# Kernel tuning notes

Measured on AMD Instinct MI355X. Metric: run time of the kernel, lower is better.

## Reference

```python
import jax, jax.numpy as jnp
import numpy as np

H, C = 4, 128            # GATConv heads, per-head out channels
MAX_NODES, NF = 50, 64   # generator graph size, node feature dim
N_NODES, N_EDGES, N_GRAPHS, LAT, HID = 10000, 160000, 64, 64, 128


def _p(key, i, shape):
    return jax.random.normal(jax.random.fold_in(key, i), shape, jnp.float32) * 0.05


def setup_inputs() -> dict:
    key = jax.random.key(0)
    inp = {}
    inp['x'] = jax.random.normal(jax.random.fold_in(key, 0), (N_NODES, NF), jnp.float32)
    inp['edge_index'] = jax.random.randint(jax.random.fold_in(key, 1), (2, N_EDGES), 0, N_NODES)
    inp['batch'] = jnp.sort(jax.random.randint(jax.random.fold_in(key, 2), (N_NODES,), 0, N_GRAPHS))
    inp['eps'] = jax.random.normal(jax.random.fold_in(key, 3), (N_GRAPHS, LAT), jnp.float32)
    # encoder params
    inp['We'] = _p(key, 10, (NF, HID)); inp['be'] = _p(key, 11, (HID,))
    inp['Wg'] = _p(key, 12, (3, HID, H * C))
    inp['ag_src'] = _p(key, 13, (3, H, C)); inp['ag_dst'] = _p(key, 14, (3, H, C))
    inp['bg'] = _p(key, 15, (3, C))
    inp['Wa1'] = _p(key, 16, (HID, 2 * HID)); inp['ba1'] = _p(key, 17, (2 * HID,))
    inp['Wa2'] = _p(key, 18, (2 * HID, HID)); inp['ba2'] = _p(key, 19, (HID,))
    inp['Wmu'] = _p(key, 20, (HID, LAT)); inp['bmu'] = _p(key, 21, (LAT,))
    inp['Wlv'] = _p(key, 22, (HID, LAT)); inp['blv'] = _p(key, 23, (LAT,))
    # generator params
    inp['Wn1'] = _p(key, 30, (LAT, 256)); inp['bn1'] = _p(key, 31, (256,))
    inp['Wn2'] = _p(key, 32, (256, 512)); inp['bn2'] = _p(key, 33, (512,))
    inp['Wn3'] = _p(key, 34, (512, MAX_NODES * NF)); inp['bn3'] = _p(key, 35, (MAX_NODES * NF,))
    inp['We1'] = _p(key, 36, (LAT + 2 * NF, 128)); inp['be1'] = _p(key, 37, (128,))
    inp['We2'] = _p(key, 38, (128, 64)); inp['be2'] = _p(key, 39, (64,))
    inp['We3'] = _p(key, 40, (64, 1)); inp['be3'] = _p(key, 41, (1,))
    inp['Wr1'] = _p(key, 42, (2 * NF, 64)); inp['br1'] = _p(key, 43, (64,))
    inp['Wr2'] = _p(key, 44, (64, 6)); inp['br2'] = _p(key, 45, (6,))
    return inp


def _gat(h, W, a_s, a_d, b, src, dst, N):
    # PyG GATConv: heads=4, concat=False (mean over heads), neg_slope=0.2, self-loops pre-added
    xh = (h @ W).reshape(N, H, C)                      # [N,H,C]
    es = (xh * a_s[None]).sum(-1)                      # [N,H] alpha_src component
    ed = (xh * a_d[None]).sum(-1)                      # [N,H] alpha_dst component
    e = jax.nn.leaky_relu(es[src] + ed[dst], 0.2)      # [E,H]
    m = jax.ops.segment_max(e, dst, num_segments=N)
    ex = jnp.exp(e - m[dst])
    den = jax.ops.segment_sum(ex, dst, num_segments=N)
    alpha = ex / den[dst]                              # softmax over incoming edges
    out = jax.ops.segment_sum(xh[src] * alpha[:, :, None], dst, num_segments=N)
    return out.mean(axis=1) + b                        # mean over heads + bias


def reference(x, eps, We, be, Wg, ag_src, ag_dst, bg, Wa1, ba1, Wa2, ba2,
              Wmu, bmu, Wlv, blv, Wn1, bn1, Wn2, bn2, Wn3, bn3,
              We1, be1, We2, be2, We3, be3, Wr1, br1, Wr2, br2,
              edge_index, batch):
    N = x.shape[0]
    B = eps.shape[0]
    loops = jnp.arange(N)
    src = jnp.concatenate([edge_index[0], loops])
    dst = jnp.concatenate([edge_index[1], loops])
    # PathwayEncoder
    h = jax.nn.relu(x @ We + be)
    for l in range(3):
        h = h + jax.nn.relu(_gat(h, Wg[l], ag_src[l], ag_dst[l], bg[l], src, dst, N))
    counts = jax.ops.segment_sum(jnp.ones((N,), h.dtype), batch, num_segments=B)
    sums = jax.ops.segment_sum(h, batch, num_segments=B)
    pr = sums / jnp.maximum(counts, 1.0)[:, None]      # global_mean_pool
    pr = jax.nn.relu(pr @ Wa1 + ba1) @ Wa2 + ba2       # pathway_aggregator
    # VAE head
    mu = pr @ Wmu + bmu
    logvar = pr @ Wlv + blv
    z = mu + eps * jnp.exp(0.5 * logvar)
    # PathwayGenerator (pairwise loop fully batched)
    g = jax.nn.relu(z @ Wn1 + bn1)
    g = jax.nn.relu(g @ Wn2 + bn2)
    nodes = (g @ Wn3 + bn3).reshape(B, MAX_NODES, NF)  # node_features (pre-sigmoid)
    node_probs = jax.nn.sigmoid(nodes)
    iu, ju = np.triu_indices(MAX_NODES, k=1)           # 1225 static pairs (i<j)
    ni = nodes[:, iu]                                  # [B,P,NF]
    nj = nodes[:, ju]
    P = iu.shape[0]
    zb = jnp.broadcast_to(z[:, None, :], (B, P, z.shape[-1]))
    eh = jax.nn.relu(jnp.concatenate([zb, ni, nj], -1) @ We1 + be1)
    eh = jax.nn.relu(eh @ We2 + be2)
    edge_probs = jax.nn.sigmoid(eh @ We3 + be3)[..., 0]            # [B,P]
    rh = jax.nn.relu(jnp.concatenate([ni, nj], -1) @ Wr1 + br1)
    reaction_types = jax.nn.softmax(rh @ Wr2 + br2, axis=-1)       # [B,P,6]
    return (mu, logvar, z, pr, node_probs, edge_probs, reaction_types)
```

## Files before the change

### kernel.cpp

```cpp
#include <hip/hip_runtime.h>
#include <cstddef>

#define N_NODES 10000
#define N_EDGES 160000
#define E_TOT   170000
#define N_GRAPHS 64
#define NF 64
#define HID 128
#define HC 512
#define LAT 64
#define MAXN 50
#define NPAIR 1225
#define NODESF 3200
#define DEG_CAP 64

typedef __attribute__((ext_vector_type(8))) short bf16x8;
typedef __attribute__((ext_vector_type(8))) unsigned short u16x8;
typedef __attribute__((ext_vector_type(4))) float f32x4;
typedef unsigned short u16;
typedef unsigned int u32;

__device__ __forceinline__ u16 f2b(float f) {
    u32 u = __float_as_uint(f);
    u32 r = (u + 0x7fffu + ((u >> 16) & 1u)) >> 16;
    return (u16)r;
}
__device__ __forceinline__ float b2f(u16 v) {
    return __uint_as_float(((u32)v) << 16);
}

struct PackArgs {
    const float* src[15];
    u16* dst[15];
};
#define PACK_TOTAL 344192
#define PACK_GRID_TOTAL (PACK_TOTAL + NPAIR + E_TOT)
__global__ void pack_all_kernel(PackArgs pa, int* __restrict__ pi, int* __restrict__ pj,
                                const int* __restrict__ ei, int* __restrict__ cursor,
                                int* __restrict__ csr_src) {
    int idx = blockIdx.x * 256 + threadIdx.x;
    if (idx >= PACK_GRID_TOTAL) return;
    if (idx >= PACK_TOTAL) {
        int r = idx - PACK_TOTAL;
        if (r < NPAIR) {
            int i = 0, off = 0;
            while (off + (MAXN - 1 - i) <= r) { off += MAXN - 1 - i; ++i; }
            pi[r] = i;
            pj[r] = i + 1 + (r - off);
        } else {
            int e = r - NPAIR;
            int s, d;
            if (e < N_EDGES) { s = ei[e]; d = ei[N_EDGES + e]; }
            else { s = e - N_EDGES; d = s; }
            int pos = atomicAdd(&cursor[d], 1);
            csr_src[(d << 6) + pos] = s;
        }
        return;
    }
    const int base[16] = {0, 8192, 16384, 24576, 27648, 28672, 29696, 33792, 37888,
                          38912, 39936, 41984, 58368, 263168, 264192, 344192};
    const int Ns[15]   = {512, 512, 512, 128, 64, 64, 256, 128, 64, 64, 256, 512, 3200, 128, 0};
    const int dNs[15]  = {512, 512, 512, 128, 64, 64, 256, 128, 128, 128, 256, 512, 3200, 128, 0};
    const int coff[15] = {0, 0, 0, 0, 0, 0, 0, 0, 0, 64, 0, 0, 0, 0, 0};
    int s = 0;
    while (idx >= base[s + 1]) ++s;
    int i = idx - base[s];
    const float* sp = pa.src[s];
    u16* dp = pa.dst[s];
    if (s == 14) {
        u16x8 o;
#pragma unroll
        for (int j = 0; j < 8; ++j) o[j] = f2b(sp[(size_t)i * 8 + j]);
        *(u16x8*)&dp[(size_t)i * 8] = o;
        return;
    }
    int N = Ns[s];
    int g = i / N, n = i - g * N;
    u16x8 o;
#pragma unroll
    for (int j = 0; j < 8; ++j) o[j] = f2b(sp[(size_t)(g * 8 + j) * N + n]);
    *(u16x8*)&dp[((size_t)g * dNs[s] + n + coff[s]) * 8] = o;
}

template<int K, int NT, int CB, bool BIAS, bool RELU, bool F32OUT>
__global__ __launch_bounds__(256) void gemm_mh_kernel(const u16* __restrict__ A,
                                                      const u16* __restrict__ Wp,
                                                      const float* __restrict__ bias,
                                                      u16* __restrict__ bo,
                                                      float* __restrict__ fo) {
    constexpr int CT = CB / 64;
    __shared__ u16 AL[64 * (K + 8)];
    int t = threadIdx.x, w = t >> 6, l = t & 63, lr = l & 15, lg = l >> 4;
    int rb = blockIdx.x * 64, j0 = blockIdx.y * CB;
    for (int u = t; u < 64 * (K / 8); u += 256) {
        int r = u / (K / 8), c8 = (u % (K / 8)) * 8;
        int row = min(rb + r, N_NODES - 1);
        *(u16x8*)&AL[r * (K + 8) + c8] = *(const u16x8*)&A[(size_t)row * K + c8];
    }
    __syncthreads();
    f32x4 acc[4][CT];
#pragma unroll
    for (int rt = 0; rt < 4; ++rt)
#pragma unroll
        for (int ct = 0; ct < CT; ++ct) acc[rt][ct] = (f32x4){0.f, 0.f, 0.f, 0.f};
#pragma unroll
    for (int ks = 0; ks < K / 32; ++ks) {
        bf16x8 a[4], b[CT];
#pragma unroll
        for (int rt = 0; rt < 4; ++rt)
            a[rt] = *(const bf16x8*)&AL[(rt * 16 + lr) * (K + 8) + ks * 32 + lg * 8];
#pragma unroll
        for (int ct = 0; ct < CT; ++ct) {
            int col = j0 + w * (CB / 4) + ct * 16 + lr;
            b[ct] = *(const bf16x8*)&Wp[(size_t)((ks * 4 + lg) * NT + col) * 8];
        }
#pragma unroll
        for (int rt = 0; rt < 4; ++rt)
#pragma unroll
            for (int ct = 0; ct < CT; ++ct)
                acc[rt][ct] = __builtin_amdgcn_mfma_f32_16x16x32_bf16(a[rt], b[ct], acc[rt][ct], 0, 0, 0);
    }
#pragma unroll
    for (int rt = 0; rt < 4; ++rt)
#pragma unroll
        for (int ct = 0; ct < CT; ++ct) {
            int col = j0 + w * (CB / 4) + ct * 16 + lr;
            float bj = BIAS ? bias[col] : 0.f;
#pragma unroll
            for (int i = 0; i < 4; ++i) {
                int row = rb + rt * 16 + lg * 4 + i;
                if (row < N_NODES) {
                    float v = acc[rt][ct][i] + bj;
                    if (RELU) v = fmaxf(v, 0.f);
                    bo[(size_t)row * NT + col] = f2b(v);
                    if (F32OUT) fo[(size_t)row * NT + col] = v;
                }
            }
        }
}

template<int K, int G, int ACT, bool SPLIT>
__global__ __launch_bounds__(256) void gemm64_kernel(const u16* __restrict__ A,
                                                     const u16* __restrict__ Wp,
                                                     const float* __restrict__ bias,
                                                     const float* __restrict__ bias2,
                                                     float* __restrict__ fo,
                                                     float* __restrict__ fo2,
                                                     u16* __restrict__ bo, int N) {
    constexpr int CG = 4 / G, NB = CG * 16, Kc = K / G, KS = Kc / 32;
    constexpr int ABYTES = 64 * (K + 8) * 2;
    constexpr int LDSB = (ABYTES > 16384) ? ABYTES : 16384;
    __shared__ float LDSf[LDSB / 4];
    u16* AL = (u16*)LDSf;
    float* RB = LDSf;
    int t = threadIdx.x, w = t >> 6, l = t & 63, lr = l & 15, lg = l >> 4;
    for (int u = t; u < 64 * (K / 8); u += 256) {
        int r = u / (K / 8), c8 = (u % (K / 8)) * 8;
        *(u16x8*)&AL[r * (K + 8) + c8] = *(const u16x8*)&A[(size_t)r * K + c8];
    }
    __syncthreads();
    int kg = w % G, cg = w / G;
    int col = blockIdx.x * NB + cg * 16 + lr;
    f32x4 acc[4];
#pragma unroll
    for (int rt = 0; rt < 4; ++rt) acc[rt] = (f32x4){0.f, 0.f, 0.f, 0.f};
#pragma unroll
    for (int ks = 0; ks < KS; ++ks) {
        int k0 = kg * Kc + ks * 32;
        bf16x8 b = *(const bf16x8*)&Wp[(size_t)(((k0 >> 3) + lg) * N + col) * 8];
#pragma unroll
        for (int rt = 0; rt < 4; ++rt) {
            bf16x8 a = *(const bf16x8*)&AL[(rt * 16 + lr) * (K + 8) + k0 + lg * 8];
            acc[rt] = __builtin_amdgcn_mfma_f32_16x16x32_bf16(a, b, acc[rt], 0, 0, 0);
        }
    }
    __syncthreads();
#pragma unroll
    for (int rt = 0; rt < 4; ++rt)
#pragma unroll
        for (int i = 0; i < 4; ++i)
            RB[w * 1024 + (rt * 16 + lg * 4 + i) * 16 + lr] = acc[rt][i];
    __syncthreads();
    for (int e = t; e < 64 * NB; e += 256) {
        int row = e / NB, cb = e - row * NB;
        int cg2 = cb >> 4, cl = cb & 15;
        float s = 0.f;
#pragma unroll
        for (int kg2 = 0; kg2 < G; ++kg2)
            s += RB[(cg2 * G + kg2) * 1024 + row * 16 + cl];
        int c = blockIdx.x * NB + cb;
        float bj;
        if (SPLIT) bj = (c < 64) ? bias[c] : bias2[c - 64];
        else bj = bias[c];
        float v = s + bj;
        if (ACT == 1) v = fmaxf(v, 0.f);
        if (bo) bo[(size_t)row * N + c] = f2b(v);
        if (SPLIT) {
            if (c < 64) fo[row * 64 + c] = v;
            else fo2[row * 64 + (c - 64)] = v;
        } else if (fo) {
            float ov = (ACT == 2) ? 1.f / (1.f + __expf(-v)) : v;
            fo[(size_t)row * N + c] = ov;
        }
    }
}

template<int K, int N, typename EP>
__device__ __forceinline__ void mm64(const u16* __restrict__ AL, int lda,
                                     const u16* __restrict__ Wp, EP ep) {
    int t = threadIdx.x, w = t >> 6, l = t & 63, lr = l & 15, lg = l >> 4;
#pragma unroll
    for (int p = 0; p < N / 64; ++p) {
        int col = p * 64 + w * 16 + lr;
        f32x4 acc[4];
#pragma unroll
        for (int rt = 0; rt < 4; ++rt) acc[rt] = (f32x4){0.f, 0.f, 0.f, 0.f};
#pragma unroll
        for (int ks = 0; ks < K / 32; ++ks) {
            bf16x8 b = *(const bf16x8*)&Wp[(size_t)((ks * 4 + lg) * N + col) * 8];
#pragma unroll
            for (int rt = 0; rt < 4; ++rt) {
                bf16x8 a = *(const bf16x8*)&AL[(rt * 16 + lr) * lda + ks * 32 + lg * 8];
                acc[rt] = __builtin_amdgcn_mfma_f32_16x16x32_bf16(a, b, acc[rt], 0, 0, 0);
            }
        }
#pragma unroll
        for (int rt = 0; rt < 4; ++rt)
#pragma unroll
            for (int i = 0; i < 4; ++i)
                ep(rt * 16 + lg * 4 + i, col, acc[rt][i]);
    }
}

__global__ __launch_bounds__(256) void fused_vae_kernel(
    const u16* __restrict__ pr0b, const float* __restrict__ eps,
    const u16* __restrict__ Wa1p, const float* __restrict__ ba1,
    const u16* __restrict__ Wa2p, const float* __restrict__ ba2,
    const u16* __restrict__ Wmulvp, const float* __restrict__ bmu, const float* __restrict__ blv,
    const u16* __restrict__ Wn1p, const float* __restrict__ bn1,
    const u16* __restrict__ Wn2p, const float* __restrict__ bn2,
    float* __restrict__ pr_o, float* __restrict__ mu_o, float* __restrict__ lv_o,
    float* __restrict__ z_o, u16* __restrict__ zbf, u16* __restrict__ g2bb) {
    __shared__ u16 P[64 * 136];
    __shared__ u16 T[64 * 272];
    __shared__ u16 Z[64 * 72];
    float* MVf = (float*)T;
    int t = threadIdx.x;
    for (int idx = t; idx < 8192; idx += 256) {
        int g = idx >> 7, c = idx & 127;
        P[g * 136 + c] = pr0b[idx];
    }
    __syncthreads();
    mm64<128, 256>(P, 136, Wa1p, [&](int row, int col, float v) {
        T[row * 272 + col] = f2b(fmaxf(v + ba1[col], 0.f));
    });
    __syncthreads();
    mm64<256, 128>(T, 272, Wa2p, [&](int row, int col, float v) {
        v += ba2[col];
        pr_o[row * 128 + col] = v;
        P[row * 136 + col] = f2b(v);
    });
    __syncthreads();
    mm64<128, 128>(P, 136, Wmulvp, [&](int row, int col, float v) {
        v += (col < 64) ? bmu[col] : blv[col - 64];
        MVf[row * 136 + col] = v;
        if (col < 64) mu_o[row * 64 + col] = v;
        else lv_o[row * 64 + (col - 64)] = v;
    });
    __syncthreads();
    for (int idx = t; idx < 4096; idx += 256) {
        int g = idx >> 6, c = idx & 63;
        float m = MVf[g * 136 + c], lvv = MVf[g * 136 + 64 + c];
        float zv = fmaf(eps[idx], __expf(0.5f * lvv), m);
        z_o[idx] = zv;
        u16 zb16 = f2b(zv);
        zbf[idx] = zb16;
        Z[g * 72 + c] = zb16;
    }
    __syncthreads();
    mm64<64, 256>(Z, 72, Wn1p, [&](int row, int col, float v) {
        T[row * 272 + col] = f2b(fmaxf(v + bn1[col], 0.f));
    });
    __syncthreads();
    mm64<256, 512>(T, 272, Wn2p, [&](int row, int col, float v) {
        g2bb[row * 512 + col] = f2b(fmaxf(v + bn2[col], 0.f));
    });
}

__global__ void esed_kernel(const u16* __restrict__ xhb, const float* __restrict__ ags,
                            const float* __restrict__ agd, float* __restrict__ es,
                            float* __restrict__ ed) {
    int wv = threadIdx.x >> 6, lane = threadIdx.x & 63;
    int n = blockIdx.x * 4 + wv;
    if (n >= N_NODES) return;
    u16x8 v = *(const u16x8*)&xhb[(size_t)n * 512 + lane * 8];
    float ps = 0.f, pd = 0.f;
#pragma unroll
    for (int j = 0; j < 8; ++j) {
        float f = b2f(v[j]);
        ps = fmaf(f, ags[lane * 8 + j], ps);
        pd = fmaf(f, agd[lane * 8 + j], pd);
    }
#pragma unroll
    for (int off = 1; off < 16; off <<= 1) {
        ps += __shfl_xor(ps, off);
        pd += __shfl_xor(pd, off);
    }
    if ((lane & 15) == 0) {
        es[n * 4 + (lane >> 4)] = ps;
        ed[n * 4 + (lane >> 4)] = pd;
    }
}

__global__ __launch_bounds__(256) void gat_agg_kernel(const u16* __restrict__ xhb,
                               const float* __restrict__ es, const float* __restrict__ ed,
                               const int* __restrict__ cursor, const int* __restrict__ csr_src,
                               const float* __restrict__ bg, float* __restrict__ h,
                               u16* __restrict__ hb) {
    __shared__ float aL[4][64][4];
    __shared__ int sL[4][64];
    int wv = threadIdx.x >> 6, lane = threadIdx.x & 63;
    int n = blockIdx.x * 4 + wv;
    int deg = cursor[n];
    const float4 ed4 = ((const float4*)ed)[n];
    const float edh[4] = {ed4.x, ed4.y, ed4.z, ed4.w};
    float ex0 = 0.f, ex1 = 0.f, ex2 = 0.f, ex3 = 0.f;
    if (lane < deg) {
        int sj = csr_src[(n << 6) + lane];
        sL[wv][lane] = sj;
        const float4 e4 = ((const float4*)es)[sj];
        const float ev[4] = {e4.x, e4.y, e4.z, e4.w};
        float exv[4];
#pragma unroll
        for (int hh = 0; hh < 4; ++hh) {
            float e = ev[hh] + edh[hh];
            e = e > 0.f ? e : 0.2f * e;
            e = fminf(e, 80.f);
            exv[hh] = __expf(e);
        }
        *(float4*)&aL[wv][lane][0] = make_float4(exv[0], exv[1], exv[2], exv[3]);
        ex0 = exv[0]; ex1 = exv[1]; ex2 = exv[2]; ex3 = exv[3];
    }
#pragma unroll
    for (int off = 32; off; off >>= 1) {
        ex0 += __shfl_xor(ex0, off);
        ex1 += __shfl_xor(ex1, off);
        ex2 += __shfl_xor(ex2, off);
        ex3 += __shfl_xor(ex3, off);
    }
    __syncthreads();
    int head = lane >> 4, c0 = (lane & 15) * 8;
    float den = (head == 0) ? ex0 : (head == 1) ? ex1 : (head == 2) ? ex2 : ex3;
    float acc[8] = {0.f, 0.f, 0.f, 0.f, 0.f, 0.f, 0.f, 0.f};
    const u16* xb_h = xhb + head * 128 + c0;
    int j2 = 0;
    for (; j2 + 2 <= deg; j2 += 2) {
        int s0 = sL[wv][j2], s1 = sL[wv][j2 + 1];
        float al0 = aL[wv][j2][head], al1 = aL[wv][j2 + 1][head];
        u16x8 v0 = *(const u16x8*)&xb_h[(size_t)s0 * 512];
        u16x8 v1 = *(const u16x8*)&xb_h[(size_t)s1 * 512];
#pragma unroll
        for (int m = 0; m < 8; ++m) acc[m] = fmaf(al0, b2f(v0[m]), acc[m]);
#pragma unroll
        for (int m = 0; m < 8; ++m) acc[m] = fmaf(al1, b2f(v1[m]), acc[m]);
    }
    if (j2 < deg) {
        int s0 = sL[wv][j2];
        float al0 = aL[wv][j2][head];
        u16x8 v0 = *(const u16x8*)&xb_h[(size_t)s0 * 512];
#pragma unroll
        for (int m = 0; m < 8; ++m) acc[m] = fmaf(al0, b2f(v0[m]), acc[m]);
    }
    float rden = 1.f / den;
#pragma unroll
    for (int m = 0; m < 8; ++m) {
        float v = acc[m] * rden;
        v += __shfl_xor(v, 16);
        v += __shfl_xor(v, 32);
        acc[m] = v;
    }
    if (lane < 16) {
        float o8[8];
        u16x8 b8;
#pragma unroll
        for (int m = 0; m < 8; ++m) {
            int c = lane * 8 + m;
            float o = acc[m] * 0.25f + bg[c];
            o = fmaxf(o, 0.f);
            float hn = h[(size_t)n * 128 + c] + o;
            o8[m] = hn;
            b8[m] = f2b(hn);
        }
        *(float4*)&h[(size_t)n * 128 + lane * 8] = make_float4(o8[0], o8[1], o8[2], o8[3]);
        *(float4*)&h[(size_t)n * 128 + lane * 8 + 4] = make_float4(o8[4], o8[5], o8[6], o8[7]);
        *(u16x8*)&hb[(size_t)n * 128 + lane * 8] = b8;
    }
}

__global__ __launch_bounds__(1024) void pool_kernel2(const float* __restrict__ h,
                                                     const int* __restrict__ batch,
                                                     u16* __restrict__ pr0b) {
    __shared__ float red[8][128];
    int g = blockIdx.x;
    int t = threadIdx.x;
    int c = t & 127, rg = t >> 7;
    int lo = 0, hi = N_NODES;
    while (lo < hi) { int m = (lo + hi) >> 1; if (batch[m] < g) lo = m + 1; else hi = m; }
    int s = lo;
    lo = 0; hi = N_NODES;
    while (lo < hi) { int m = (lo + hi) >> 1; if (batch[m] < g + 1) lo = m + 1; else hi = m; }
    int e = lo;
    float acc = 0.f;
    for (int n = s + rg; n < e; n += 8) acc += h[(size_t)n * HID + c];
    red[rg][c] = acc;
    __syncthreads();
    if (rg == 0) {
        float sum = ((red[0][c] + red[1][c]) + (red[2][c] + red[3][c])) +
                    ((red[4][c] + red[5][c]) + (red[6][c] + red[7][c]));
        float cn = fmaxf((float)(e - s), 1.f);
        pr0b[g * HID + c] = f2b(sum / cn);
    }
}

__global__ __launch_bounds__(256) void edge_react_mfma(
    const u16* __restrict__ zb, const u16* __restrict__ nb,
    const int* __restrict__ pi, const int* __restrict__ pj,
    const u16* __restrict__ We1p, const float* __restrict__ be1,
    const u16* __restrict__ We2p, const float* __restrict__ be2,
    const float* __restrict__ We3, const float* __restrict__ be3,
    const u16* __restrict__ Wr1p, const float* __restrict__ br1,
    const float* __restrict__ Wr2, const float* __restrict__ br2,
    float* __restrict__ edgep, float* __restrict__ react) {
    __shared__ u16 inA[64 * 200];
    __shared__ u16 h1A[64 * 136];
    __shared__ u16 rhA[64 * 68];
    int t = threadIdx.x, w = t >> 6, l = t & 63, lr = l & 15, lg = l >> 4;
    int b = blockIdx.y, p0 = blockIdx.x * 64;
    for (int u = t; u < 1536; u += 256) {
        int r = u / 24, c8 = (u % 24) * 8;
        int p = min(p0 + r, NPAIR - 1);
        const u16* src;
        if (c8 < 64) src = zb + b * 64 + c8;
        else if (c8 < 128) src = nb + b * NODESF + pi[p] * 64 + (c8 - 64);
        else src = nb + b * NODESF + pj[p] * 64 + (c8 - 128);
        *(u16x8*)&inA[r * 200 + c8] = *(const u16x8*)src;
    }
    __syncthreads();
    f32x4 a1[4][2];
#pragma unroll
    for (int rt = 0; rt < 4; ++rt)
#pragma unroll
        for (int ct = 0; ct < 2; ++ct) a1[rt][ct] = (f32x4){0.f, 0.f, 0.f, 0.f};
#pragma unroll
    for (int ks = 0; ks < 6; ++ks) {
        bf16x8 af[4], bf_[2];
#pragma unroll
        for (int rt = 0; rt < 4; ++rt)
            af[rt] = *(const bf16x8*)&inA[(rt * 16 + lr) * 200 + ks * 32 + lg * 8];
#pragma unroll
        for (int ct = 0; ct < 2; ++ct) {
            int col = w * 32 + ct * 16 + lr;
            bf_[ct] = *(const bf16x8*)&We1p[(size_t)((ks * 4 + lg) * 128 + col) * 8];
        }
#pragma unroll
        for (int rt = 0; rt < 4; ++rt)
#pragma unroll
            for (int ct = 0; ct < 2; ++ct)
                a1[rt][ct] = __builtin_amdgcn_mfma_f32_16x16x32_bf16(af[rt], bf_[ct], a1[rt][ct], 0, 0, 0);
    }
    f32x4 r1[4];
#pragma unroll
    for (int rt = 0; rt < 4; ++rt) r1[rt] = (f32x4){0.f, 0.f, 0.f, 0.f};
#pragma unroll
    for (int ks = 0; ks < 4; ++ks) {
        bf16x8 af[4];
#pragma unroll
        for (int rt = 0; rt < 4; ++rt)
            af[rt] = *(const bf16x8*)&inA[(rt * 16 + lr) * 200 + 64 + ks * 32 + lg * 8];
        int col = w * 16 + lr;
        bf16x8 bf_ = *(const bf16x8*)&Wr1p[(size_t)((ks * 4 + lg) * 64 + col) * 8];
#pragma unroll
        for (int rt = 0; rt < 4; ++rt)
            r1[rt] = __builtin_amdgcn_mfma_f32_16x16x32_bf16(af[rt], bf_, r1[rt], 0, 0, 0);
    }
#pragma unroll
    for (int rt = 0; rt < 4; ++rt)
#pragma unroll
        for (int ct = 0; ct < 2; ++ct) {
            int col = w * 32 + ct * 16 + lr;
            float bia = be1[col];
#pragma unroll
            for (int i = 0; i < 4; ++i) {
                int row = rt * 16 + lg * 4 + i;
                h1A[row * 136 + col] = f2b(fmaxf(a1[rt][ct][i] + bia, 0.f));
            }
        }
#pragma unroll
    for (int rt = 0; rt < 4; ++rt) {
        int col = w * 16 + lr;
        float bia = br1[col];
#pragma unroll
        for (int i = 0; i < 4; ++i) {
            int row = rt * 16 + lg * 4 + i;
            rhA[row * 68 + col] = f2b(fmaxf(r1[rt][i] + bia, 0.f));
        }
    }
    __syncthreads();
    f32x4 a2[4];
#pragma unroll
    for (int rt = 0; rt < 4; ++rt) a2[rt] = (f32x4){0.f, 0.f, 0.f, 0.f};
#pragma unroll
    for (int ks = 0; ks < 4; ++ks) {
        bf16x8 af[4];
#pragma unroll
        for (int rt = 0; rt < 4; ++rt)
            af[rt] = *(const bf16x8*)&h1A[(rt * 16 + lr) * 136 + ks * 32 + lg * 8];
        int col = w * 16 + lr;
        bf16x8 bf_ = *(const bf16x8*)&We2p[(size_t)((ks * 4 + lg) * 64 + col) * 8];
#pragma unroll
        for (int rt = 0; rt < 4; ++rt)
            a2[rt] = __builtin_amdgcn_mfma_f32_16x16x32_bf16(af[rt], bf_, a2[rt], 0, 0, 0);
    }
    u16* h2A = inA;
#pragma unroll
    for (int rt = 0; rt < 4; ++rt) {
        int col = w * 16 + lr;
        float bia = be2[col];
#pragma unroll
        for (int i = 0; i < 4; ++i) {
            int row = rt * 16 + lg * 4 + i;
            h2A[row * 68 + col] = f2b(fmaxf(a2[rt][i] + bia, 0.f));
        }
    }
    __syncthreads();
    int r = t >> 2, sub = t & 3;
    int p = p0 + r;
    float acc3 = 0.f;
#pragma unroll
    for (int kk = 0; kk < 16; ++kk) {
        int c = sub * 16 + kk;
        acc3 = fmaf(b2f(h2A[r * 68 + c]), We3[c], acc3);
    }
    acc3 += __shfl_xor(acc3, 1);
    acc3 += __shfl_xor(acc3, 2);
    if (sub == 0 && p < NPAIR)
        edgep[b * NPAIR + p] = 1.f / (1.f + __expf(-(acc3 + be3[0])));
    float lg6[6] = {0.f, 0.f, 0.f, 0.f, 0.f, 0.f};
#pragma unroll
    for (int kk = 0; kk < 16; ++kk) {
        int c = sub * 16 + kk;
        float v = b2f(rhA[r * 68 + c]);
#pragma unroll
        for (int m = 0; m < 6; ++m) lg6[m] = fmaf(v, Wr2[c * 6 + m], lg6[m]);
    }
#pragma unroll
    for (int m = 0; m < 6; ++m) {
        lg6[m] += __shfl_xor(lg6[m], 1);
        lg6[m] += __shfl_xor(lg6[m], 2);
    }
    if (sub == 0 && p < NPAIR) {
        float mx = -3.4e38f;
#pragma unroll
        for (int m = 0; m < 6; ++m) { lg6[m] += br2[m]; mx = fmaxf(mx, lg6[m]); }
        float s = 0.f;
        float ex[6];
#pragma unroll
        for (int m = 0; m < 6; ++m) { ex[m] = __expf(lg6[m] - mx); s += ex[m]; }
        float rs = 1.f / s;
#pragma unroll
        for (int m = 0; m < 6; ++m) react[(size_t)(b * NPAIR + p) * 6 + m] = ex[m] * rs;
    }
}

extern "C" void kernel_launch(void* const* d_in, const int* in_sizes, int n_in,
                              void* d_out, int out_size, void* d_ws, size_t ws_size,
                              hipStream_t stream) {
    const float* x     = (const float*)d_in[0];
    const int*   ei    = (const int*)d_in[1];
    const int*   batch = (const int*)d_in[2];
    const float* eps   = (const float*)d_in[3];
    const float* We    = (const float*)d_in[4];
    const float* be    = (const float*)d_in[5];
    const float* Wg    = (const float*)d_in[6];
    const float* ags   = (const float*)d_in[7];
    const float* agd   = (const float*)d_in[8];
    const float* bg    = (const float*)d_in[9];
    const float* Wa1   = (const float*)d_in[10];
    const float* ba1   = (const float*)d_in[11];
    const float* Wa2   = (const float*)d_in[12];
    const float* ba2   = (const float*)d_in[13];
    const float* Wmu   = (const float*)d_in[14];
    const float* bmu   = (const float*)d_in[15];
    const float* Wlv   = (const float*)d_in[16];
    const float* blv   = (const float*)d_in[17];
    const float* Wn1   = (const float*)d_in[18];
    const float* bn1   = (const float*)d_in[19];
    const float* Wn2   = (const float*)d_in[20];
    const float* bn2   = (const float*)d_in[21];
    const float* Wn3   = (const float*)d_in[22];
    const float* bn3   = (const float*)d_in[23];
    const float* We1   = (const float*)d_in[24];
    const float* be1   = (const float*)d_in[25];
    const float* We2   = (const float*)d_in[26];
    const float* be2   = (const float*)d_in[27];
    const float* We3   = (const float*)d_in[28];
    const float* be3   = (const float*)d_in[29];
    const float* Wr1   = (const float*)d_in[30];
    const float* br1   = (const float*)d_in[31];
    const float* Wr2   = (const float*)d_in[32];
    const float* br2   = (const float*)d_in[33];

    float* out = (float*)d_out;
    float* mu_o    = out;
    float* lv_o    = out + 4096;
    float* z_o     = out + 8192;
    float* pr_o    = out + 12288;
    float* nodep_o = out + 20480;
    float* edgep_o = out + 225280;
    float* react_o = out + 303680;

    float* F = (float*)d_ws;
    size_t o = 0;
    float* h  = F + o; o += (size_t)N_NODES * HID;
    float* es = F + o; o += (size_t)N_NODES * 4;
    float* ed = F + o; o += (size_t)N_NODES * 4;
    u16* U = (u16*)(F + o);
    size_t uo = 0;
    u16* hb     = U + uo; uo += (size_t)N_NODES * HID;
    u16* xb     = U + uo; uo += (size_t)N_NODES * NF;
    u16* xhb    = U + uo; uo += (size_t)N_NODES * HC;
    u16* zbf    = U + uo; uo += 4096;
    u16* nbf    = U + uo; uo += 64 * NODESF;
    u16* pr0b   = U + uo; uo += 64 * HID;
    u16* g2bb   = U + uo; uo += 64 * 512;
    u16* Wgp    = U + uo; uo += (size_t)3 * 16 * 512 * 8;
    u16* We1p   = U + uo; uo += 24 * 128 * 8;
    u16* We2p   = U + uo; uo += 16 * 64 * 8;
    u16* Wr1p   = U + uo; uo += 16 * 64 * 8;
    u16* Wa1p   = U + uo; uo += 16 * 256 * 8;
    u16* Wa2p   = U + uo; uo += 32 * 128 * 8;
    u16* Wmulvp = U + uo; uo += 16 * 128 * 8;
    u16* Wn1p   = U + uo; uo += 8 * 256 * 8;
    u16* Wn2p   = U + uo; uo += 32 * 512 * 8;
    u16* Wn3p   = U + uo; uo += (size_t)64 * 3200 * 8;
    u16* Wep    = U + uo; uo += 8 * 128 * 8;
    if (uo & 7) uo += 8 - (uo & 7);
    int* I = (int*)(U + uo);
    int* piA     = I;
    int* pjA     = piA + NPAIR;
    int* cursor  = pjA + NPAIR;
    int* csr_src = cursor + N_NODES;

    hipMemsetAsync(cursor, 0, (size_t)N_NODES * sizeof(int), stream);

    PackArgs pa;
    pa.src[0] = Wg;               pa.dst[0] = Wgp;
    pa.src[1] = Wg + 65536;       pa.dst[1] = Wgp + 65536;
    pa.src[2] = Wg + 131072;      pa.dst[2] = Wgp + 131072;
    pa.src[3] = We1;              pa.dst[3] = We1p;
    pa.src[4] = We2;              pa.dst[4] = We2p;
    pa.src[5] = Wr1;              pa.dst[5] = Wr1p;
    pa.src[6] = Wa1;              pa.dst[6] = Wa1p;
    pa.src[7] = Wa2;              pa.dst[7] = Wa2p;
    pa.src[8] = Wmu;              pa.dst[8] = Wmulvp;
    pa.src[9] = Wlv;              pa.dst[9] = Wmulvp;
    pa.src[10] = Wn1;             pa.dst[10] = Wn1p;
    pa.src[11] = Wn2;             pa.dst[11] = Wn2p;
    pa.src[12] = Wn3;             pa.dst[12] = Wn3p;
    pa.src[13] = We;              pa.dst[13] = Wep;
    pa.src[14] = x;               pa.dst[14] = xb;
    pack_all_kernel<<<(PACK_GRID_TOTAL + 255) / 256, 256, 0, stream>>>(
        pa, piA, pjA, ei, cursor, csr_src);

    gemm_mh_kernel<64, 128, 128, true, true, true>
        <<<dim3((N_NODES + 63) / 64, 1), 256, 0, stream>>>(xb, Wep, be, hb, h);

    for (int l = 0; l < 3; ++l) {
        gemm_mh_kernel<128, 512, 64, false, false, false>
            <<<dim3((N_NODES + 63) / 64, 8), 256, 0, stream>>>(
                hb, Wgp + (size_t)l * 65536, nullptr, xhb, nullptr);
        esed_kernel<<<N_NODES / 4, 256, 0, stream>>>(xhb, ags + l * HC, agd + l * HC, es, ed);
        gat_agg_kernel<<<N_NODES / 4, 256, 0, stream>>>(xhb, es, ed, cursor, csr_src,
                                                        bg + l * HID, h, hb);
    }

    pool_kernel2<<<N_GRAPHS, 1024, 0, stream>>>(h, batch, pr0b);

    fused_vae_kernel<<<1, 256, 0, stream>>>(
        pr0b, eps, Wa1p, ba1, Wa2p, ba2, Wmulvp, bmu, blv,
        Wn1p, bn1, Wn2p, bn2, pr_o, mu_o, lv_o, z_o, zbf, g2bb);

    gemm64_kernel<512, 4, 2, false><<<200, 256, 0, stream>>>(
        g2bb, Wn3p, bn3, nullptr, nodep_o, nullptr, nbf, 3200);

    edge_react_mfma<<<dim3(20, 64), 256, 0, stream>>>(
        zbf, nbf, piA, pjA, We1p, be1, We2p, be2, We3, be3,
        Wr1p, br1, Wr2, br2, edgep_o, react_o);
}
```

Before: 220.4 us.

## Fold attention vectors into weights and fuse es/ed into aggregation epilogue

Precomputes W_g·a_src and W_g·a_dst per layer and head in the pack kernel, so the attention logits can be computed directly from the 128-wide hidden state instead of the 512-wide projected features. The first layer's logits come from a small new kernel. Later layers' logits are computed in the GAT aggregation epilogue from the fp32 residual output, with es/ed buffers double-buffered across layers. This removes three esed launches and their re-read of xhb. The trade-off is a change in rounding (fp32 h instead of bf16 xh for later layers, though layer 0 uses bf16 hb) and extra epilogue work in the aggregation kernel.

```diff
diff --git a/kernel.cpp b/kernel.cpp
--- a/kernel.cpp
+++ b/kernel.cpp
@@ -34,10 +34,13 @@
     u16* dst[15];
 };
 #define PACK_TOTAL 344192
-#define PACK_GRID_TOTAL (PACK_TOTAL + NPAIR + E_TOT)
+#define PACK_W 3072
+#define PACK_GRID_TOTAL (PACK_TOTAL + NPAIR + E_TOT + PACK_W)
 __global__ void pack_all_kernel(PackArgs pa, int* __restrict__ pi, int* __restrict__ pj,
                                 const int* __restrict__ ei, int* __restrict__ cursor,
-                                int* __restrict__ csr_src) {
+                                int* __restrict__ csr_src,
+                                const float* __restrict__ Wg, const float* __restrict__ ags,
+                                const float* __restrict__ agd, float* __restrict__ wesed) {
     int idx = blockIdx.x * 256 + threadIdx.x;
     if (idx >= PACK_GRID_TOTAL) return;
     if (idx >= PACK_TOTAL) {
@@ -47,13 +50,23 @@
             while (off + (MAXN - 1 - i) <= r) { off += MAXN - 1 - i; ++i; }
             pi[r] = i;
             pj[r] = i + 1 + (r - off);
-        } else {
+        } else if (r < NPAIR + E_TOT) {
             int e = r - NPAIR;
             int s, d;
             if (e < N_EDGES) { s = ei[e]; d = ei[N_EDGES + e]; }
             else { s = e - N_EDGES; d = s; }
             int pos = atomicAdd(&cursor[d], 1);
             csr_src[(d << 6) + pos] = s;
+        } else {
+            int i = r - NPAIR - E_TOT;
+            int l = i >> 10, rr = i & 1023;
+            int sd = rr >> 9, hh = (rr >> 7) & 3, k = rr & 127;
+            const float* wrow = Wg + ((size_t)(l * 128 + k)) * 512 + hh * 128;
+            const float* ag = (sd ? agd : ags) + (l * 4 + hh) * 128;
+            float s = 0.f;
+#pragma unroll 8
+            for (int c = 0; c < 128; ++c) s = fmaf(wrow[c], ag[c], s);
+            wesed[(l * 8 + sd * 4 + hh) * 128 + k] = s;
         }
         return;
     }
@@ -287,48 +300,57 @@
     });
 }
 
-__global__ void esed_kernel(const u16* __restrict__ xhb, const float* __restrict__ ags,
-                            const float* __restrict__ agd, float* __restrict__ es,
-                            float* __restrict__ ed) {
-    int wv = threadIdx.x >> 6, lane = threadIdx.x & 63;
-    int n = blockIdx.x * 4 + wv;
-    if (n >= N_NODES) return;
-    u16x8 v = *(const u16x8*)&xhb[(size_t)n * 512 + lane * 8];
-    float ps = 0.f, pd = 0.f;
-#pragma unroll
-    for (int j = 0; j < 8; ++j) {
-        float f = b2f(v[j]);
-        ps = fmaf(f, ags[lane * 8 + j], ps);
-        pd = fmaf(f, agd[lane * 8 + j], pd);
-    }
-#pragma unroll
-    for (int off = 1; off < 16; off <<= 1) {
-        ps += __shfl_xor(ps, off);
-        pd += __shfl_xor(pd, off);
-    }
-    if ((lane & 15) == 0) {
-        es[n * 4 + (lane >> 4)] = ps;
-        ed[n * 4 + (lane >> 4)] = pd;
+__global__ __launch_bounds__(256) void esed0_kernel(const u16* __restrict__ hb,
+                                                    const float* __restrict__ w,
+                                                    float* __restrict__ es,
+                                                    float* __restrict__ ed) {
+    int t = threadIdx.x;
+    int wv = t >> 6, lane = t & 63;
+    int g16 = lane >> 4, l16 = lane & 15;
+    int n = blockIdx.x * 16 + wv * 4 + g16;
+    u16x8 v = *(const u16x8*)&hb[(size_t)n * 128 + l16 * 8];
+    float ch[8];
+#pragma unroll
+    for (int j = 0; j < 8; ++j) ch[j] = b2f(v[j]);
+    float p[8];
+#pragma unroll
+    for (int o = 0; o < 8; ++o) {
+        const float* wo = w + o * 128 + l16 * 8;
+        float s = 0.f;
+#pragma unroll
+        for (int j = 0; j < 8; ++j) s = fmaf(ch[j], wo[j], s);
+        p[o] = s;
+    }
+#pragma unroll
+    for (int o = 0; o < 8; ++o) {
+#pragma unroll
+        for (int m = 1; m < 16; m <<= 1) p[o] += __shfl_xor(p[o], m);
+    }
+    if (l16 < 8) {
+        if (l16 < 4) es[n * 4 + l16] = p[l16];
+        else ed[n * 4 + (l16 - 4)] = p[l16];
     }
 }
 
 __global__ __launch_bounds__(256) void gat_agg_kernel(const u16* __restrict__ xhb,
-                               const float* __restrict__ es, const float* __restrict__ ed,
+                               const float* __restrict__ es_in, const float* __restrict__ ed_in,
                                const int* __restrict__ cursor, const int* __restrict__ csr_src,
                                const float* __restrict__ bg, float* __restrict__ h,
-                               u16* __restrict__ hb) {
+                               u16* __restrict__ hb,
+                               const float* __restrict__ w_next,
+                               float* __restrict__ es_out, float* __restrict__ ed_out) {
     __shared__ float aL[4][64][4];
     __shared__ int sL[4][64];
     int wv = threadIdx.x >> 6, lane = threadIdx.x & 63;
     int n = blockIdx.x * 4 + wv;
     int deg = cursor[n];
-    const float4 ed4 = ((const float4*)ed)[n];
+    const float4 ed4 = ((const float4*)ed_in)[n];
     const float edh[4] = {ed4.x, ed4.y, ed4.z, ed4.w};
     float ex0 = 0.f, ex1 = 0.f, ex2 = 0.f, ex3 = 0.f;
     if (lane < deg) {
         int sj = csr_src[(n << 6) + lane];
         sL[wv][lane] = sj;
-        const float4 e4 = ((const float4*)es)[sj];
+        const float4 e4 = ((const float4*)es_in)[sj];
         const float ev[4] = {e4.x, e4.y, e4.z, e4.w};
         float exv[4];
 #pragma unroll
@@ -394,6 +416,26 @@
         *(float4*)&h[(size_t)n * 128 + lane * 8] = make_float4(o8[0], o8[1], o8[2], o8[3]);
         *(float4*)&h[(size_t)n * 128 + lane * 8 + 4] = make_float4(o8[4], o8[5], o8[6], o8[7]);
         *(u16x8*)&hb[(size_t)n * 128 + lane * 8] = b8;
+        if (w_next) {
+            float p[8];
+#pragma unroll
+            for (int o = 0; o < 8; ++o) {
+                const float* wo = w_next + o * 128 + lane * 8;
+                float s = 0.f;
+#pragma unroll
+                for (int j = 0; j < 8; ++j) s = fmaf(o8[j], wo[j], s);
+                p[o] = s;
+            }
+#pragma unroll
+            for (int o = 0; o < 8; ++o) {
+#pragma unroll
+                for (int m = 1; m < 16; m <<= 1) p[o] += __shfl_xor(p[o], m);
+            }
+            if (lane < 8) {
+                if (lane < 4) es_out[n * 4 + lane] = p[lane];
+                else ed_out[n * 4 + (lane - 4)] = p[lane];
+            }
+        }
     }
 }
 
@@ -621,9 +663,12 @@
 
     float* F = (float*)d_ws;
     size_t o = 0;
-    float* h  = F + o; o += (size_t)N_NODES * HID;
-    float* es = F + o; o += (size_t)N_NODES * 4;
-    float* ed = F + o; o += (size_t)N_NODES * 4;
+    float* h   = F + o; o += (size_t)N_NODES * HID;
+    float* es0 = F + o; o += (size_t)N_NODES * 4;
+    float* ed0 = F + o; o += (size_t)N_NODES * 4;
+    float* es1 = F + o; o += (size_t)N_NODES * 4;
+    float* ed1 = F + o; o += (size_t)N_NODES * 4;
+    float* wesed = F + o; o += PACK_W;
     u16* U = (u16*)(F + o);
     size_t uo = 0;
     u16* hb     = U + uo; uo += (size_t)N_NODES * HID;
@@ -670,18 +715,24 @@
     pa.src[13] = We;              pa.dst[13] = Wep;
     pa.src[14] = x;               pa.dst[14] = xb;
     pack_all_kernel<<<(PACK_GRID_TOTAL + 255) / 256, 256, 0, stream>>>(
-        pa, piA, pjA, ei, cursor, csr_src);
+        pa, piA, pjA, ei, cursor, csr_src, Wg, ags, agd, wesed);
 
     gemm_mh_kernel<64, 128, 128, true, true, true>
         <<<dim3((N_NODES + 63) / 64, 1), 256, 0, stream>>>(xb, Wep, be, hb, h);
 
+    esed0_kernel<<<N_NODES / 16, 256, 0, stream>>>(hb, wesed, es0, ed0);
+
+    float* esA = es0; float* edA = ed0;
+    float* esB = es1; float* edB = ed1;
     for (int l = 0; l < 3; ++l) {
         gemm_mh_kernel<128, 512, 64, false, false, false>
             <<<dim3((N_NODES + 63) / 64, 8), 256, 0, stream>>>(
                 hb, Wgp + (size_t)l * 65536, nullptr, xhb, nullptr);
-        esed_kernel<<<N_NODES / 4, 256, 0, stream>>>(xhb, ags + l * HC, agd + l * HC, es, ed);
-        gat_agg_kernel<<<N_NODES / 4, 256, 0, stream>>>(xhb, es, ed, cursor, csr_src,
-                                                        bg + l * HID, h, hb);
+        const float* w_next = (l < 2) ? (wesed + (size_t)(l + 1) * 1024) : nullptr;
+        gat_agg_kernel<<<N_NODES / 4, 256, 0, stream>>>(
+            xhb, esA, edA, cursor, csr_src, bg + l * HID, h, hb, w_next, esB, edB);
+        float* te = esA; esA = esB; esB = te;
+        float* td = edA; edA = edB; edB = td;
     }
 
     pool_kernel2<<<N_GRAPHS, 1024, 0, stream>>>(h, batch, pr0b);
```

After: 235.4 us, median of 2. +6.8%, slower.
